# Optimization experiments

Hardware: AMD Instinct MI355X
Metric: run time of the kernel (lower is better)

## Reference

```python
import jax, jax.numpy as jnp
import numpy as np

D = 2048           # model dim
E = 8              # num experts
K = 2              # top_k
H = int(D * 8 / 3) # SwiGLU hidden dim (5461), matches torch default
B, S = 2, 2048


def setup_inputs() -> dict:
    key = jax.random.key(0)
    ks = jax.random.split(key, 5)
    x = jax.random.normal(ks[0], (B, S, D), jnp.float32)
    wg = jax.random.normal(ks[1], (E, D), jnp.float32) * 0.02   # gate Linear weight [out,in]
    w1 = jax.random.normal(ks[2], (E, H, D), jnp.float32) * 0.02  # per-expert w1 [H,D]
    w2 = jax.random.normal(ks[3], (E, D, H), jnp.float32) * 0.02  # per-expert w2 [D,H]
    w3 = jax.random.normal(ks[4], (E, H, D), jnp.float32) * 0.02  # per-expert w3 [H,D]
    return {"x": x, "wg": wg, "w1": w1, "w2": w2, "w3": w3}


def reference(x, wg, w1, w2, w3):
    b, s, d = x.shape
    xf = x.reshape(-1, d)                         # [T, D]
    T = xf.shape[0]

    # --- gating (eval mode: no noise) ---
    logits = xf @ wg.T                            # [T, E]
    topk_vals, topk_idx = jax.lax.top_k(logits, K)  # [T, K]
    topk_probs = jax.nn.softmax(topk_vals, axis=-1)  # softmax over the K selected
    gate_probs = jax.nn.softmax(logits, axis=-1)     # [T, E] for load-balancing loss
    mean_probs = gate_probs.mean(axis=0)             # [E]
    # torch .std() is unbiased (ddof=1)
    lb_loss = (jnp.std(mean_probs, ddof=1) / (mean_probs.mean() + 1e-10)) ** 2

    # --- combine weights: scatter top-k probs into dense [T, E] ---
    cw = jnp.zeros((T, E), xf.dtype).at[jnp.arange(T)[:, None], topk_idx].add(topk_probs)

    # --- per-expert SwiGLU over all tokens (dense grouped GEMMs) ---
    h = jax.nn.silu(jnp.einsum('td,ehd->eth', xf, w1)) * jnp.einsum('td,ehd->eth', xf, w3)
    ye = jnp.einsum('eth,edh->etd', h, w2)        # [E, T, D]

    # --- weighted combine ---
    out = jnp.einsum('etd,te->td', ye, cw).reshape(b, s, d)
    return out, 0.01 * lb_loss
```

## Files before the change

### kernel.cpp

```cpp
#include <hip/hip_runtime.h>
#include <hip/hip_bf16.h>

#define Tn 4096
#define Dm 2048
#define En 8
#define Hh 5461
#define HP 5504

typedef __attribute__((ext_vector_type(8))) short bf16x8;
typedef __attribute__((ext_vector_type(4))) float f32x4;

__device__ __forceinline__ unsigned short f2bf(float f) {
  union { __hip_bfloat16 b; unsigned short u; } c;
  c.b = __float2bfloat16(f);
  return c.u;
}

__device__ __forceinline__ uint4 pack8(const float* f) {
  union { unsigned short us[8]; uint4 v; } o;
#pragma unroll
  for (int i = 0; i < 8; ++i) o.us[i] = f2bf(f[i]);
  return o.v;
}

__device__ __forceinline__ void gl16(const void* g, void* lds) {
  __builtin_amdgcn_global_load_lds(
      (const __attribute__((address_space(1))) unsigned int*)g,
      (__attribute__((address_space(3))) unsigned int*)lds, 16, 0, 0);
}

#define WAIT8_BAR() asm volatile("s_waitcnt vmcnt(8)\n\ts_barrier" ::: "memory")
#define WAIT6_BAR() asm volatile("s_waitcnt vmcnt(6)\n\ts_barrier" ::: "memory")
#define WAIT0_BAR() asm volatile("s_waitcnt vmcnt(0)\n\ts_barrier" ::: "memory")
#define LGK0_BAR()  asm volatile("s_waitcnt lgkmcnt(0)\n\ts_barrier" ::: "memory")


__global__ __launch_bounds__(64) void gating_kernel(
    const float* __restrict__ x, const float* __restrict__ wg,
    float* __restrict__ gate_p, int* __restrict__ topk_e, float* __restrict__ topk_p,
    unsigned short* __restrict__ xb)
{
  const int t = blockIdx.x;
  const int l = threadIdx.x;
  const float* xr = x + (size_t)t * Dm;
  float acc[En];
#pragma unroll
  for (int e = 0; e < En; ++e) acc[e] = 0.f;
  for (int d = l; d < Dm; d += 64) {
    const float xv = xr[d];
#pragma unroll
    for (int e = 0; e < En; ++e) acc[e] = fmaf(xv, wg[e * Dm + d], acc[e]);
  }
#pragma unroll
  for (int e = 0; e < En; ++e) {
    float v = acc[e];
#pragma unroll
    for (int s = 32; s > 0; s >>= 1) v += __shfl_xor(v, s);
    acc[e] = v;
  }
  unsigned short* xrow = xb + (size_t)t * Dm;
#pragma unroll
  for (int k = 0; k < 4; ++k) {
    const int b = k * 512 + l * 8;
    float f[8];
    *(float4*)(f)     = *(const float4*)(xr + b);
    *(float4*)(f + 4) = *(const float4*)(xr + b + 4);
    *(uint4*)(xrow + b) = pack8(f);
  }
  if (l == 0) {
    float m = acc[0];
    for (int e = 1; e < En; ++e) m = fmaxf(m, acc[e]);
    float p[En]; float s = 0.f;
    for (int e = 0; e < En; ++e) { p[e] = __expf(acc[e] - m); s += p[e]; }
    const float inv = 1.f / s;
    for (int e = 0; e < En; ++e) gate_p[t * En + e] = p[e] * inv;
    int e0 = 0; float v0 = acc[0];
    for (int e = 1; e < En; ++e) if (acc[e] > v0) { v0 = acc[e]; e0 = e; }
    int e1 = -1; float v1 = -3.4e38f;
    for (int e = 0; e < En; ++e) if (e != e0 && acc[e] > v1) { v1 = acc[e]; e1 = e; }
    const float q  = __expf(v1 - v0);
    const float q0 = 1.f / (1.f + q);
    const float q1 = q * q0;
    topk_e[t * 2] = e0; topk_e[t * 2 + 1] = e1;
    topk_p[t * 2] = q0; topk_p[t * 2 + 1] = q1;
  }
}

__global__ __launch_bounds__(256) void reduce_scatter_kernel(
    const int* __restrict__ topk_e, const float* __restrict__ topk_p,
    const float* __restrict__ gate_p,
    int* __restrict__ counts, int* __restrict__ offs,
    int* __restrict__ pair_token, int* __restrict__ slot_of,
    float* __restrict__ out_scalar)
{
  __shared__ int cnt_s[En];
  __shared__ int run_s[En];
  __shared__ float red[256 * En];
  const int tid = threadIdx.x;
  if (tid < En) cnt_s[tid] = 0;
  __syncthreads();
  for (int i = tid; i < Tn * 2; i += 256) atomicAdd(&cnt_s[topk_e[i]], 1);
  __syncthreads();
  if (tid == 0) {
    int o = 0;
    for (int e = 0; e < En; ++e) {
      offs[e] = o; run_s[e] = o; counts[e] = cnt_s[e]; o += cnt_s[e];
    }
  }
  __syncthreads();
  for (int i = tid; i < Tn * 2; i += 256) {
    const int e = topk_e[i];
    const int slot = atomicAdd(&run_s[e], 1);
    pair_token[slot] = i >> 1;
    slot_of[i] = slot;
  }
  float p8[En];
#pragma unroll
  for (int e = 0; e < En; ++e) p8[e] = 0.f;
  for (int t = tid; t < Tn; t += 256)
#pragma unroll
    for (int e = 0; e < En; ++e) p8[e] += gate_p[t * En + e];
#pragma unroll
  for (int e = 0; e < En; ++e) red[tid * En + e] = p8[e];
  __syncthreads();
  for (int s = 128; s > 0; s >>= 1) {
    if (tid < s)
#pragma unroll
      for (int e = 0; e < En; ++e) red[tid * En + e] += red[(tid + s) * En + e];
    __syncthreads();
  }
  if (tid == 0) {
    double mp[En]; double sum = 0.0;
    for (int e = 0; e < En; ++e) { mp[e] = (double)red[e] / (double)Tn; sum += mp[e]; }
    const double mean = sum / En;
    double var = 0.0;
    for (int e = 0; e < En; ++e) { const double d = mp[e] - mean; var += d * d; }
    var /= (En - 1);
    const double denom = mean + 1e-10;
    *out_scalar = (float)(0.01 * var / (denom * denom));
  }
}

__global__ __launch_bounds__(256) void cvt_w13_kernel(
    const float* __restrict__ w1, const float* __restrict__ w3,
    unsigned short* __restrict__ w1b, unsigned short* __restrict__ w3b)
{
  const float* src = blockIdx.y ? w3 : w1;
  unsigned short* dst = blockIdx.y ? w3b : w1b;
  const unsigned i = ((unsigned)blockIdx.x * 256u + threadIdx.x) * 8u;
  const unsigned per_e = (unsigned)HP * Dm;
  const unsigned e = i / per_e;
  const unsigned r = i % per_e;
  const unsigned row = r / Dm, col = r % Dm;
  uint4 v;
  if (row < Hh) {
    const float* s = src + (size_t)e * Hh * Dm + (size_t)row * Dm + col;
    float f[8];
    *(float4*)(f)     = *(const float4*)(s);
    *(float4*)(f + 4) = *(const float4*)(s + 4);
    v = pack8(f);
  } else {
    v = (uint4){0, 0, 0, 0};
  }
  *(uint4*)(dst + i) = v;
}

__global__ __launch_bounds__(256) void cvt_w2_kernel(const float* __restrict__ w2,
                                                     unsigned short* __restrict__ w2b)
{
  const unsigned i = ((unsigned)blockIdx.x * 256u + threadIdx.x) * 8u;
  const unsigned per_e = (unsigned)Dm * HP;
  const unsigned e = i / per_e;
  const unsigned r = i % per_e;
  const unsigned row = r / HP, col = r % HP;
  const float* s = w2 + (size_t)e * Dm * Hh + (size_t)row * Hh + col;
  float f[8];
#pragma unroll
  for (int k = 0; k < 8; ++k) f[k] = (col + k < Hh) ? s[k] : 0.f;
  *(uint4*)(w2b + i) = pack8(f);
}

__global__ __launch_bounds__(256, 2) void gemm1_kernel(
    const unsigned short* __restrict__ xb,
    const unsigned short* __restrict__ w1b, const unsigned short* __restrict__ w3b,
    const int* __restrict__ counts, const int* __restrict__ offs,
    const int* __restrict__ pair_token,
    unsigned short* __restrict__ h)
{
  const int bid = blockIdx.x;
  const int logical = (bid & 7) * 344 + (bid >> 3);
  const int z  = logical & 7;
  const int pe = logical >> 3;
  const int e  = pe & 7;
  const int jp = pe >> 3;

  const int cnt = counts[e];
  if (cnt <= 0) return;
  const int base = offs[e];
  const int j0 = jp * 128;
  const int tid = threadIdx.x;
  const int l = tid & 63;
  const int wid = tid >> 6;
  const int wr = wid >> 1, wc = wid & 1;

  __shared__ unsigned short As[2][128 * 32];
  __shared__ unsigned short B1[2][128 * 32];
  __shared__ unsigned short B3[2][128 * 32];

  const int r0 = tid >> 2;
  const int r1 = 64 + (tid >> 2);
  const int c0 = (((tid & 3) ^ ((tid >> 3) & 3))) * 8;
  const int wb0 = wid * 512;
  const int wb1 = 2048 + wid * 512;

  const unsigned short* b1r0 = w1b + ((size_t)e * HP + j0 + r0) * Dm + c0;
  const unsigned short* b1r1 = w1b + ((size_t)e * HP + j0 + r1) * Dm + c0;
  const unsigned short* b3r0 = w3b + ((size_t)e * HP + j0 + r0) * Dm + c0;
  const unsigned short* b3r1 = w3b + ((size_t)e * HP + j0 + r1) * Dm + c0;

  const int lr = l & 15;
  const int sq = (((l >> 4) ^ ((lr >> 1) & 3))) * 8;

#define STAGE1(b, kk) do { \
    gl16(a0 + (kk), &As[b][wb0]);   gl16(a1 + (kk), &As[b][wb1]); \
    gl16(b1r0 + (kk), &B1[b][wb0]); gl16(b1r1 + (kk), &B1[b][wb1]); \
    gl16(b3r0 + (kk), &B3[b][wb0]); gl16(b3r1 + (kk), &B3[b][wb1]); \
  } while (0)

#define COMPUTE1(b) do { \
    bf16x8 av[4], b1v[4], b3v[4]; \
    _Pragma("unroll") \
    for (int m = 0; m < 4; ++m) \
      av[m] = *(const bf16x8*)(&As[b][(wr * 64 + m * 16 + lr) * 32 + sq]); \
    _Pragma("unroll") \
    for (int n = 0; n < 4; ++n) { \
      b1v[n] = *(const bf16x8*)(&B1[b][(wc * 64 + n * 16 + lr) * 32 + sq]); \
      b3v[n] = *(const bf16x8*)(&B3[b][(wc * 64 + n * 16 + lr) * 32 + sq]); \
    } \
    _Pragma("unroll") \
    for (int m = 0; m < 4; ++m) \
      _Pragma("unroll") \
      for (int n = 0; n < 4; ++n) { \
        acc1[m][n] = __builtin_amdgcn_mfma_f32_16x16x32_bf16(av[m], b1v[n], acc1[m][n], 0, 0, 0); \
        acc3[m][n] = __builtin_amdgcn_mfma_f32_16x16x32_bf16(av[m], b3v[n], acc3[m][n], 0, 0, 0); \
      } \
  } while (0)

  for (int mt = z; mt * 128 < cnt; mt += 8) {
    const int row0 = mt * 128;
    int s0 = row0 + r0; if (s0 >= cnt) s0 = cnt - 1;
    int s1 = row0 + r1; if (s1 >= cnt) s1 = cnt - 1;
    const unsigned short* a0 = xb + (size_t)pair_token[base + s0] * Dm + c0;
    const unsigned short* a1 = xb + (size_t)pair_token[base + s1] * Dm + c0;

    f32x4 acc1[4][4], acc3[4][4];
#pragma unroll
    for (int m = 0; m < 4; ++m)
#pragma unroll
      for (int n = 0; n < 4; ++n) {
        acc1[m][n] = (f32x4){0.f, 0.f, 0.f, 0.f};
        acc3[m][n] = (f32x4){0.f, 0.f, 0.f, 0.f};
      }

    STAGE1(0, 0);
    int cur = 0;
    for (int kk = 0; kk < Dm - 32; kk += 32) {
      STAGE1(cur ^ 1, kk + 32);
      WAIT6_BAR();
      COMPUTE1(cur);
      LGK0_BAR();
      cur ^= 1;
    }
    WAIT0_BAR();
    COMPUTE1(cur);
    LGK0_BAR();

#pragma unroll
    for (int m = 0; m < 4; ++m) {
      const int rb = wr * 64 + m * 16 + ((l >> 4) << 2);
#pragma unroll
      for (int i = 0; i < 4; ++i) {
        const int sl2 = row0 + rb + i;
        if (sl2 < cnt) {
          unsigned short* hrow = h + (size_t)(base + sl2) * HP + j0 + wc * 64 + lr;
#pragma unroll
          for (int n = 0; n < 4; ++n) {
            const float aa = acc1[m][n][i];
            const float g = aa / (1.f + __expf(-aa));
            hrow[n * 16] = f2bf(g * acc3[m][n][i]);
          }
        }
      }
    }
  }
#undef STAGE1
#undef COMPUTE1
}

__global__ __launch_bounds__(256, 2) void gemm2_kernel(
    const unsigned short* __restrict__ h, const unsigned short* __restrict__ w2b,
    const int* __restrict__ counts, const int* __restrict__ offs,
    float* __restrict__ y)
{
  const int bid = blockIdx.x;
  const int logical = (bid & 7) * 128 + (bid >> 3);
  const int z  = logical & 7;
  const int pe = logical >> 3;
  const int e  = pe & 7;
  const int dp = pe >> 3;

  const int cnt = counts[e];
  if (cnt <= 0) return;
  const int base = offs[e];
  const int d0 = dp * 128;
  const int tid = threadIdx.x;
  const int l = tid & 63;
  const int wid = tid >> 6;
  const int wr = wid >> 1, wc = wid & 1;

  __shared__ unsigned short Ah[2][128 * 64];
  __shared__ unsigned short Bs[2][128 * 64];

  const int r0 = tid >> 3;
  const int c0 = (((tid & 7) ^ ((tid >> 3) & 7))) * 8;

  const unsigned short* br0 = w2b + ((size_t)e * Dm + d0 + r0)      * HP + c0;
  const unsigned short* br1 = w2b + ((size_t)e * Dm + d0 + r0 + 32) * HP + c0;
  const unsigned short* br2 = w2b + ((size_t)e * Dm + d0 + r0 + 64) * HP + c0;
  const unsigned short* br3 = w2b + ((size_t)e * Dm + d0 + r0 + 96) * HP + c0;

  const int wbA0 = (0 * 256 + wid * 64) * 8;
  const int wbA1 = (1 * 256 + wid * 64) * 8;
  const int wbA2 = (2 * 256 + wid * 64) * 8;
  const int wbA3 = (3 * 256 + wid * 64) * 8;

  const int lr = l & 15;
  const int sq0 = (((0 * 4 + (l >> 4)) ^ (lr & 7))) * 8;
  const int sq1 = (((1 * 4 + (l >> 4)) ^ (lr & 7))) * 8;

#define STAGE2(b, kk) do { \
    gl16(a0 + (kk), &Ah[b][wbA0]); gl16(a1 + (kk), &Ah[b][wbA1]); \
    gl16(a2 + (kk), &Ah[b][wbA2]); gl16(a3 + (kk), &Ah[b][wbA3]); \
    gl16(br0 + (kk), &Bs[b][wbA0]); gl16(br1 + (kk), &Bs[b][wbA1]); \
    gl16(br2 + (kk), &Bs[b][wbA2]); gl16(br3 + (kk), &Bs[b][wbA3]); \
  } while (0)

#define COMPUTE2(b) do { \
    bf16x8 av[4], bv[4]; \
    _Pragma("unroll") \
    for (int m = 0; m < 4; ++m) \
      av[m] = *(const bf16x8*)(&Ah[b][(wr * 64 + m * 16 + lr) * 64 + sq0]); \
    _Pragma("unroll") \
    for (int n = 0; n < 4; ++n) \
      bv[n] = *(const bf16x8*)(&Bs[b][(wc * 64 + n * 16 + lr) * 64 + sq0]); \
    _Pragma("unroll") \
    for (int m = 0; m < 4; ++m) \
      _Pragma("unroll") \
      for (int n = 0; n < 4; ++n) \
        acc[m][n] = __builtin_amdgcn_mfma_f32_16x16x32_bf16(av[m], bv[n], acc[m][n], 0, 0, 0); \
    _Pragma("unroll") \
    for (int m = 0; m < 4; ++m) \
      av[m] = *(const bf16x8*)(&Ah[b][(wr * 64 + m * 16 + lr) * 64 + sq1]); \
    _Pragma("unroll") \
    for (int n = 0; n < 4; ++n) \
      bv[n] = *(const bf16x8*)(&Bs[b][(wc * 64 + n * 16 + lr) * 64 + sq1]); \
    _Pragma("unroll") \
    for (int m = 0; m < 4; ++m) \
      _Pragma("unroll") \
      for (int n = 0; n < 4; ++n) \
        acc[m][n] = __builtin_amdgcn_mfma_f32_16x16x32_bf16(av[m], bv[n], acc[m][n], 0, 0, 0); \
  } while (0)

  for (int mt = z; mt * 128 < cnt; mt += 8) {
    const int row0 = mt * 128;
    int s0 = row0 + r0;      if (s0 >= cnt) s0 = cnt - 1;
    int s1 = row0 + r0 + 32; if (s1 >= cnt) s1 = cnt - 1;
    int s2 = row0 + r0 + 64; if (s2 >= cnt) s2 = cnt - 1;
    int s3 = row0 + r0 + 96; if (s3 >= cnt) s3 = cnt - 1;
    const unsigned short* a0 = h + (size_t)(base + s0) * HP + c0;
    const unsigned short* a1 = h + (size_t)(base + s1) * HP + c0;
    const unsigned short* a2 = h + (size_t)(base + s2) * HP + c0;
    const unsigned short* a3 = h + (size_t)(base + s3) * HP + c0;

    f32x4 acc[4][4];
#pragma unroll
    for (int m = 0; m < 4; ++m)
#pragma unroll
      for (int n = 0; n < 4; ++n) acc[m][n] = (f32x4){0.f, 0.f, 0.f, 0.f};

    STAGE2(0, 0);
    int cur = 0;
    for (int kk = 0; kk < HP - 64; kk += 64) {
      STAGE2(cur ^ 1, kk + 64);
      WAIT8_BAR();
      COMPUTE2(cur);
      LGK0_BAR();
      cur ^= 1;
    }
    WAIT0_BAR();
    COMPUTE2(cur);
    LGK0_BAR();

#pragma unroll
    for (int m = 0; m < 4; ++m) {
      const int rb = row0 + wr * 64 + m * 16 + ((l >> 4) << 2);
#pragma unroll
      for (int i = 0; i < 4; ++i) {
        const int sl2 = rb + i;
        if (sl2 < cnt) {
          float* yrow = y + (size_t)(base + sl2) * Dm + d0 + wc * 64 + lr;
#pragma unroll
          for (int n = 0; n < 4; ++n)
            yrow[n * 16] = acc[m][n][i];
        }
      }
    }
  }
#undef STAGE2
#undef COMPUTE2
}

__global__ __launch_bounds__(256) void combine_kernel(
    const float* __restrict__ y, const int* __restrict__ slot_of,
    const float* __restrict__ topk_p, float* __restrict__ out)
{
  const int t = blockIdx.x;
  const int s0 = slot_of[t * 2], s1 = slot_of[t * 2 + 1];
  const float w0 = topk_p[t * 2], w1 = topk_p[t * 2 + 1];
  const float* y0 = y + (size_t)s0 * Dm;
  const float* y1 = y + (size_t)s1 * Dm;
  float* o = out + (size_t)t * Dm;
  const int c = threadIdx.x * 8;
  float4 a0 = *(const float4*)(y0 + c);
  float4 a1 = *(const float4*)(y0 + c + 4);
  float4 b0 = *(const float4*)(y1 + c);
  float4 b1 = *(const float4*)(y1 + c + 4);
  float4 r0, r1;
  r0.x = w0 * a0.x + w1 * b0.x; r0.y = w0 * a0.y + w1 * b0.y;
  r0.z = w0 * a0.z + w1 * b0.z; r0.w = w0 * a0.w + w1 * b0.w;
  r1.x = w0 * a1.x + w1 * b1.x; r1.y = w0 * a1.y + w1 * b1.y;
  r1.z = w0 * a1.z + w1 * b1.z; r1.w = w0 * a1.w + w1 * b1.w;
  *(float4*)(o + c) = r0;
  *(float4*)(o + c + 4) = r1;
}

extern "C" void kernel_launch(void* const* d_in, const int* in_sizes, int n_in,
                              void* d_out, int out_size, void* d_ws, size_t ws_size,
                              hipStream_t stream) {
  const float* x  = (const float*)d_in[0];
  const float* wg = (const float*)d_in[1];
  const float* w1 = (const float*)d_in[2];
  const float* w2 = (const float*)d_in[3];
  const float* w3 = (const float*)d_in[4];
  float* out = (float*)d_out;

  char* ws = (char*)d_ws;
  int*    counts     = (int*)(ws + 64);
  int*    offs       = (int*)(ws + 128);
  int*    topk_e     = (int*)(ws + 1024);
  float*  topk_p     = (float*)(ws + 40960);
  int*    pair_token = (int*)(ws + 81920);
  float*  gate_p     = (float*)(ws + 163840);
  int*    slot_of    = (int*)(ws + 307200);
  const size_t MB = 1u << 20;
  unsigned short* xb  = (unsigned short*)(ws + 1 * MB);
  unsigned short* h   = (unsigned short*)(ws + 17 * MB);
  unsigned short* w1b = (unsigned short*)(ws + 104 * MB);
  unsigned short* w3b = (unsigned short*)(ws + 276 * MB);
  unsigned short* w2b = (unsigned short*)(ws + 448 * MB);
  float* y = (float*)(ws + 104 * MB);

  gating_kernel  <<<Tn, 64, 0, stream>>>(x, wg, gate_p, topk_e, topk_p, xb);
  reduce_scatter_kernel<<<1, 256, 0, stream>>>(topk_e, topk_p, gate_p, counts, offs,
                                               pair_token, slot_of, out + (size_t)Tn * Dm);
  cvt_w13_kernel <<<dim3(En * HP * Dm / 8 / 256, 2), 256, 0, stream>>>(w1, w3, w1b, w3b);
  cvt_w2_kernel  <<<En * Dm * HP / 8 / 256, 256, 0, stream>>>(w2, w2b);
  gemm1_kernel   <<<43 * En * 8, 256, 0, stream>>>(xb, w1b, w3b, counts, offs, pair_token, h);
  gemm2_kernel   <<<(Dm / 128) * En * 8, 256, 0, stream>>>(h, w2b, counts, offs, y);
  combine_kernel <<<Tn, 256, 0, stream>>>(y, slot_of, topk_p, out);
}
```

Before: 1.464 ms.

## Restructure gemm1 into 8-wave 256-row tiles with triple-buffered phased MFMA schedule

gemm1 moves from 4 waves on a 128x128 tile to 8 waves on a 256x128 tile, so each loaded weight tile is reused across twice as many token rows. The shared-memory pipeline goes from double to triple buffering with a two-stage prefetch. Each k-step is split into four phases of LDS reads and MFMAs separated by barriers, with s_setprio raising priority around the MFMA bursts so waves interleave memory and matrix work. The cost is more LDS per block, more barriers per k-step and fewer blocks in the grid, which can hurt occupancy and load balance across experts with uneven token counts.

```diff
diff --git a/kernel.cpp b/kernel.cpp
--- a/kernel.cpp
+++ b/kernel.cpp
@@ -31,8 +31,11 @@
 
 #define WAIT8_BAR() asm volatile("s_waitcnt vmcnt(8)\n\ts_barrier" ::: "memory")
 #define WAIT6_BAR() asm volatile("s_waitcnt vmcnt(6)\n\ts_barrier" ::: "memory")
+#define WAIT4_BAR() asm volatile("s_waitcnt vmcnt(4)\n\ts_barrier" ::: "memory")
 #define WAIT0_BAR() asm volatile("s_waitcnt vmcnt(0)\n\ts_barrier" ::: "memory")
 #define LGK0_BAR()  asm volatile("s_waitcnt lgkmcnt(0)\n\ts_barrier" ::: "memory")
+#define BAR_LGK0()  asm volatile("s_barrier\n\ts_waitcnt lgkmcnt(0)" ::: "memory")
+#define BARP()      asm volatile("s_barrier" ::: "memory")
 
 
 __global__ __launch_bounds__(64) void gating_kernel(
@@ -180,7 +183,7 @@
   *(uint4*)(w2b + i) = pack8(f);
 }
 
-__global__ __launch_bounds__(256, 2) void gemm1_kernel(
+__global__ __launch_bounds__(512, 2) void gemm1_kernel(
     const unsigned short* __restrict__ xb,
     const unsigned short* __restrict__ w1b, const unsigned short* __restrict__ w3b,
     const int* __restrict__ counts, const int* __restrict__ offs,
@@ -188,9 +191,9 @@
     unsigned short* __restrict__ h)
 {
   const int bid = blockIdx.x;
-  const int logical = (bid & 7) * 344 + (bid >> 3);
-  const int z  = logical & 7;
-  const int pe = logical >> 3;
+  const int logical = (bid & 7) * 172 + (bid >> 3);
+  const int z  = logical & 3;
+  const int pe = logical >> 2;
   const int e  = pe & 7;
   const int jp = pe >> 3;
 
@@ -201,57 +204,99 @@
   const int tid = threadIdx.x;
   const int l = tid & 63;
   const int wid = tid >> 6;
-  const int wr = wid >> 1, wc = wid & 1;
-
-  __shared__ unsigned short As[2][128 * 32];
-  __shared__ unsigned short B1[2][128 * 32];
-  __shared__ unsigned short B3[2][128 * 32];
+  const int wr = wid & 3;
+  const int wc = wid >> 2;
+
+  __shared__ unsigned short As[3][256 * 32];
+  __shared__ unsigned short B1s[3][128 * 32];
+  __shared__ unsigned short B3s[3][128 * 32];
 
   const int r0 = tid >> 2;
-  const int r1 = 64 + (tid >> 2);
   const int c0 = (((tid & 3) ^ ((tid >> 3) & 3))) * 8;
-  const int wb0 = wid * 512;
-  const int wb1 = 2048 + wid * 512;
-
-  const unsigned short* b1r0 = w1b + ((size_t)e * HP + j0 + r0) * Dm + c0;
-  const unsigned short* b1r1 = w1b + ((size_t)e * HP + j0 + r1) * Dm + c0;
-  const unsigned short* b3r0 = w3b + ((size_t)e * HP + j0 + r0) * Dm + c0;
-  const unsigned short* b3r1 = w3b + ((size_t)e * HP + j0 + r1) * Dm + c0;
+  const int wbA0 = wid * 512;
+  const int wbA1 = 4096 + wid * 512;
+  const int wbB  = wid * 512;
+
+  const unsigned short* b1g = w1b + ((size_t)e * HP + j0 + r0) * Dm + c0;
+  const unsigned short* b3g = w3b + ((size_t)e * HP + j0 + r0) * Dm + c0;
 
   const int lr = l & 15;
   const int sq = (((l >> 4) ^ ((lr >> 1) & 3))) * 8;
 
-#define STAGE1(b, kk) do { \
-    gl16(a0 + (kk), &As[b][wb0]);   gl16(a1 + (kk), &As[b][wb1]); \
-    gl16(b1r0 + (kk), &B1[b][wb0]); gl16(b1r1 + (kk), &B1[b][wb1]); \
-    gl16(b3r0 + (kk), &B3[b][wb0]); gl16(b3r1 + (kk), &B3[b][wb1]); \
+#define STG(b, kk) do { \
+    gl16(a0g + (kk), &As[b][wbA0]); gl16(a1g + (kk), &As[b][wbA1]); \
+    gl16(b1g + (kk), &B1s[b][wbB]); gl16(b3g + (kk), &B3s[b][wbB]); \
   } while (0)
 
-#define COMPUTE1(b) do { \
-    bf16x8 av[4], b1v[4], b3v[4]; \
-    _Pragma("unroll") \
-    for (int m = 0; m < 4; ++m) \
-      av[m] = *(const bf16x8*)(&As[b][(wr * 64 + m * 16 + lr) * 32 + sq]); \
-    _Pragma("unroll") \
-    for (int n = 0; n < 4; ++n) { \
-      b1v[n] = *(const bf16x8*)(&B1[b][(wc * 64 + n * 16 + lr) * 32 + sq]); \
-      b3v[n] = *(const bf16x8*)(&B3[b][(wc * 64 + n * 16 + lr) * 32 + sq]); \
-    } \
-    _Pragma("unroll") \
-    for (int m = 0; m < 4; ++m) \
-      _Pragma("unroll") \
-      for (int n = 0; n < 4; ++n) { \
-        acc1[m][n] = __builtin_amdgcn_mfma_f32_16x16x32_bf16(av[m], b1v[n], acc1[m][n], 0, 0, 0); \
-        acc3[m][n] = __builtin_amdgcn_mfma_f32_16x16x32_bf16(av[m], b3v[n], acc3[m][n], 0, 0, 0); \
-      } \
+#define PHASES(b) do { \
+    bf16x8 av0 = *(const bf16x8*)(&As[b][(wr * 64 +  0 + lr) * 32 + sq]); \
+    bf16x8 av1 = *(const bf16x8*)(&As[b][(wr * 64 + 16 + lr) * 32 + sq]); \
+    bf16x8 av2 = *(const bf16x8*)(&As[b][(wr * 64 + 32 + lr) * 32 + sq]); \
+    bf16x8 av3 = *(const bf16x8*)(&As[b][(wr * 64 + 48 + lr) * 32 + sq]); \
+    bf16x8 t0 = *(const bf16x8*)(&B1s[b][(wc * 64 +  0 + lr) * 32 + sq]); \
+    bf16x8 t1 = *(const bf16x8*)(&B1s[b][(wc * 64 + 16 + lr) * 32 + sq]); \
+    BAR_LGK0(); \
+    __builtin_amdgcn_s_setprio(1); \
+    acc1[0][0] = __builtin_amdgcn_mfma_f32_16x16x32_bf16(av0, t0, acc1[0][0], 0, 0, 0); \
+    acc1[1][0] = __builtin_amdgcn_mfma_f32_16x16x32_bf16(av1, t0, acc1[1][0], 0, 0, 0); \
+    acc1[2][0] = __builtin_amdgcn_mfma_f32_16x16x32_bf16(av2, t0, acc1[2][0], 0, 0, 0); \
+    acc1[3][0] = __builtin_amdgcn_mfma_f32_16x16x32_bf16(av3, t0, acc1[3][0], 0, 0, 0); \
+    acc1[0][1] = __builtin_amdgcn_mfma_f32_16x16x32_bf16(av0, t1, acc1[0][1], 0, 0, 0); \
+    acc1[1][1] = __builtin_amdgcn_mfma_f32_16x16x32_bf16(av1, t1, acc1[1][1], 0, 0, 0); \
+    acc1[2][1] = __builtin_amdgcn_mfma_f32_16x16x32_bf16(av2, t1, acc1[2][1], 0, 0, 0); \
+    acc1[3][1] = __builtin_amdgcn_mfma_f32_16x16x32_bf16(av3, t1, acc1[3][1], 0, 0, 0); \
+    __builtin_amdgcn_s_setprio(0); \
+    BARP(); \
+    t0 = *(const bf16x8*)(&B3s[b][(wc * 64 +  0 + lr) * 32 + sq]); \
+    t1 = *(const bf16x8*)(&B3s[b][(wc * 64 + 16 + lr) * 32 + sq]); \
+    BAR_LGK0(); \
+    __builtin_amdgcn_s_setprio(1); \
+    acc3[0][0] = __builtin_amdgcn_mfma_f32_16x16x32_bf16(av0, t0, acc3[0][0], 0, 0, 0); \
+    acc3[1][0] = __builtin_amdgcn_mfma_f32_16x16x32_bf16(av1, t0, acc3[1][0], 0, 0, 0); \
+    acc3[2][0] = __builtin_amdgcn_mfma_f32_16x16x32_bf16(av2, t0, acc3[2][0], 0, 0, 0); \
+    acc3[3][0] = __builtin_amdgcn_mfma_f32_16x16x32_bf16(av3, t0, acc3[3][0], 0, 0, 0); \
+    acc3[0][1] = __builtin_amdgcn_mfma_f32_16x16x32_bf16(av0, t1, acc3[0][1], 0, 0, 0); \
+    acc3[1][1] = __builtin_amdgcn_mfma_f32_16x16x32_bf16(av1, t1, acc3[1][1], 0, 0, 0); \
+    acc3[2][1] = __builtin_amdgcn_mfma_f32_16x16x32_bf16(av2, t1, acc3[2][1], 0, 0, 0); \
+    acc3[3][1] = __builtin_amdgcn_mfma_f32_16x16x32_bf16(av3, t1, acc3[3][1], 0, 0, 0); \
+    __builtin_amdgcn_s_setprio(0); \
+    BARP(); \
+    t0 = *(const bf16x8*)(&B1s[b][(wc * 64 + 32 + lr) * 32 + sq]); \
+    t1 = *(const bf16x8*)(&B1s[b][(wc * 64 + 48 + lr) * 32 + sq]); \
+    BAR_LGK0(); \
+    __builtin_amdgcn_s_setprio(1); \
+    acc1[0][2] = __builtin_amdgcn_mfma_f32_16x16x32_bf16(av0, t0, acc1[0][2], 0, 0, 0); \
+    acc1[1][2] = __builtin_amdgcn_mfma_f32_16x16x32_bf16(av1, t0, acc1[1][2], 0, 0, 0); \
+    acc1[2][2] = __builtin_amdgcn_mfma_f32_16x16x32_bf16(av2, t0, acc1[2][2], 0, 0, 0); \
+    acc1[3][2] = __builtin_amdgcn_mfma_f32_16x16x32_bf16(av3, t0, acc1[3][2], 0, 0, 0); \
+    acc1[0][3] = __builtin_amdgcn_mfma_f32_16x16x32_bf16(av0, t1, acc1[0][3], 0, 0, 0); \
+    acc1[1][3] = __builtin_amdgcn_mfma_f32_16x16x32_bf16(av1, t1, acc1[1][3], 0, 0, 0); \
+    acc1[2][3] = __builtin_amdgcn_mfma_f32_16x16x32_bf16(av2, t1, acc1[2][3], 0, 0, 0); \
+    acc1[3][3] = __builtin_amdgcn_mfma_f32_16x16x32_bf16(av3, t1, acc1[3][3], 0, 0, 0); \
+    __builtin_amdgcn_s_setprio(0); \
+    BARP(); \
+    t0 = *(const bf16x8*)(&B3s[b][(wc * 64 + 32 + lr) * 32 + sq]); \
+    t1 = *(const bf16x8*)(&B3s[b][(wc * 64 + 48 + lr) * 32 + sq]); \
+    BAR_LGK0(); \
+    __builtin_amdgcn_s_setprio(1); \
+    acc3[0][2] = __builtin_amdgcn_mfma_f32_16x16x32_bf16(av0, t0, acc3[0][2], 0, 0, 0); \
+    acc3[1][2] = __builtin_amdgcn_mfma_f32_16x16x32_bf16(av1, t0, acc3[1][2], 0, 0, 0); \
+    acc3[2][2] = __builtin_amdgcn_mfma_f32_16x16x32_bf16(av2, t0, acc3[2][2], 0, 0, 0); \
+    acc3[3][2] = __builtin_amdgcn_mfma_f32_16x16x32_bf16(av3, t0, acc3[3][2], 0, 0, 0); \
+    acc3[0][3] = __builtin_amdgcn_mfma_f32_16x16x32_bf16(av0, t1, acc3[0][3], 0, 0, 0); \
+    acc3[1][3] = __builtin_amdgcn_mfma_f32_16x16x32_bf16(av1, t1, acc3[1][3], 0, 0, 0); \
+    acc3[2][3] = __builtin_amdgcn_mfma_f32_16x16x32_bf16(av2, t1, acc3[2][3], 0, 0, 0); \
+    acc3[3][3] = __builtin_amdgcn_mfma_f32_16x16x32_bf16(av3, t1, acc3[3][3], 0, 0, 0); \
+    __builtin_amdgcn_s_setprio(0); \
+    BARP(); \
   } while (0)
 
-  for (int mt = z; mt * 128 < cnt; mt += 8) {
-    const int row0 = mt * 128;
-    int s0 = row0 + r0; if (s0 >= cnt) s0 = cnt - 1;
-    int s1 = row0 + r1; if (s1 >= cnt) s1 = cnt - 1;
-    const unsigned short* a0 = xb + (size_t)pair_token[base + s0] * Dm + c0;
-    const unsigned short* a1 = xb + (size_t)pair_token[base + s1] * Dm + c0;
+  for (int mt = z; mt * 256 < cnt; mt += 4) {
+    const int row0 = mt * 256;
+    int s0 = row0 + r0;       if (s0 >= cnt) s0 = cnt - 1;
+    int s1 = row0 + 128 + r0; if (s1 >= cnt) s1 = cnt - 1;
+    const unsigned short* a0g = xb + (size_t)pair_token[base + s0] * Dm + c0;
+    const unsigned short* a1g = xb + (size_t)pair_token[base + s1] * Dm + c0;
 
     f32x4 acc1[4][4], acc3[4][4];
 #pragma unroll
@@ -262,18 +307,21 @@
         acc3[m][n] = (f32x4){0.f, 0.f, 0.f, 0.f};
       }
 
-    STAGE1(0, 0);
+    STG(0, 0);
+    STG(1, 32);
     int cur = 0;
-    for (int kk = 0; kk < Dm - 32; kk += 32) {
-      STAGE1(cur ^ 1, kk + 32);
-      WAIT6_BAR();
-      COMPUTE1(cur);
-      LGK0_BAR();
-      cur ^= 1;
+    for (int t = 0; t < 62; ++t) {
+      int sb = cur + 2; if (sb >= 3) sb -= 3;
+      STG(sb, (t + 2) * 32);
+      WAIT8_BAR();
+      PHASES(cur);
+      cur = (cur == 2) ? 0 : cur + 1;
     }
+    WAIT4_BAR();
+    PHASES(cur);
+    cur = (cur == 2) ? 0 : cur + 1;
     WAIT0_BAR();
-    COMPUTE1(cur);
-    LGK0_BAR();
+    PHASES(cur);
 
 #pragma unroll
     for (int m = 0; m < 4; ++m) {
@@ -293,8 +341,8 @@
       }
     }
   }
-#undef STAGE1
-#undef COMPUTE1
+#undef STG
+#undef PHASES
 }
 
 __global__ __launch_bounds__(256, 2) void gemm2_kernel(
@@ -475,7 +523,7 @@
                                                pair_token, slot_of, out + (size_t)Tn * Dm);
   cvt_w13_kernel <<<dim3(En * HP * Dm / 8 / 256, 2), 256, 0, stream>>>(w1, w3, w1b, w3b);
   cvt_w2_kernel  <<<En * Dm * HP / 8 / 256, 256, 0, stream>>>(w2, w2b);
-  gemm1_kernel   <<<43 * En * 8, 256, 0, stream>>>(xb, w1b, w3b, counts, offs, pair_token, h);
+  gemm1_kernel   <<<43 * En * 4, 512, 0, stream>>>(xb, w1b, w3b, counts, offs, pair_token, h);
   gemm2_kernel   <<<(Dm / 128) * En * 8, 256, 0, stream>>>(h, w2b, counts, offs, y);
   combine_kernel <<<Tn, 256, 0, stream>>>(y, slot_of, topk_p, out);
 }
```

Result: slower. 1.695 ms (+15.8%).

## Fuse w1/w3 bf16 conversion into gemm1 by staging fp32 weights in LDS

Applied to the files above, without the earlier changes.

Drops the separate kernel that converted w1 and w3 from fp32 to padded bf16 copies. gemm1 now streams the fp32 weights straight into LDS with swizzled global-to-LDS loads and converts them to bf16 while building the MFMA fragments. Padded hidden columns are zeroed at the h store instead. This removes a full pass that read both fp32 weight tensors and wrote their bf16 copies. In exchange gemm1 fetches twice as many weight bytes per tile, uses more LDS (which may limit occupancy), and spends extra VALU work on conversion in its inner loop.

```diff
diff --git a/kernel.cpp b/kernel.cpp
--- a/kernel.cpp
+++ b/kernel.cpp
@@ -23,16 +23,23 @@
   return o.v;
 }
 
+__device__ __forceinline__ bf16x8 cvt8(float4 a, float4 b) {
+  union { unsigned short us[8]; bf16x8 v; } o;
+  o.us[0] = f2bf(a.x); o.us[1] = f2bf(a.y); o.us[2] = f2bf(a.z); o.us[3] = f2bf(a.w);
+  o.us[4] = f2bf(b.x); o.us[5] = f2bf(b.y); o.us[6] = f2bf(b.z); o.us[7] = f2bf(b.w);
+  return o.v;
+}
+
 __device__ __forceinline__ void gl16(const void* g, void* lds) {
   __builtin_amdgcn_global_load_lds(
       (const __attribute__((address_space(1))) unsigned int*)g,
       (__attribute__((address_space(3))) unsigned int*)lds, 16, 0, 0);
 }
 
-#define WAIT8_BAR() asm volatile("s_waitcnt vmcnt(8)\n\ts_barrier" ::: "memory")
-#define WAIT6_BAR() asm volatile("s_waitcnt vmcnt(6)\n\ts_barrier" ::: "memory")
-#define WAIT0_BAR() asm volatile("s_waitcnt vmcnt(0)\n\ts_barrier" ::: "memory")
-#define LGK0_BAR()  asm volatile("s_waitcnt lgkmcnt(0)\n\ts_barrier" ::: "memory")
+#define WAIT10_BAR() asm volatile("s_waitcnt vmcnt(10)\n\ts_barrier" ::: "memory")
+#define WAIT8_BAR()  asm volatile("s_waitcnt vmcnt(8)\n\ts_barrier" ::: "memory")
+#define WAIT0_BAR()  asm volatile("s_waitcnt vmcnt(0)\n\ts_barrier" ::: "memory")
+#define LGK0_BAR()   asm volatile("s_waitcnt lgkmcnt(0)\n\ts_barrier" ::: "memory")
 
 
 __global__ __launch_bounds__(64) void gating_kernel(
@@ -141,30 +148,6 @@
   }
 }
 
-__global__ __launch_bounds__(256) void cvt_w13_kernel(
-    const float* __restrict__ w1, const float* __restrict__ w3,
-    unsigned short* __restrict__ w1b, unsigned short* __restrict__ w3b)
-{
-  const float* src = blockIdx.y ? w3 : w1;
-  unsigned short* dst = blockIdx.y ? w3b : w1b;
-  const unsigned i = ((unsigned)blockIdx.x * 256u + threadIdx.x) * 8u;
-  const unsigned per_e = (unsigned)HP * Dm;
-  const unsigned e = i / per_e;
-  const unsigned r = i % per_e;
-  const unsigned row = r / Dm, col = r % Dm;
-  uint4 v;
-  if (row < Hh) {
-    const float* s = src + (size_t)e * Hh * Dm + (size_t)row * Dm + col;
-    float f[8];
-    *(float4*)(f)     = *(const float4*)(s);
-    *(float4*)(f + 4) = *(const float4*)(s + 4);
-    v = pack8(f);
-  } else {
-    v = (uint4){0, 0, 0, 0};
-  }
-  *(uint4*)(dst + i) = v;
-}
-
 __global__ __launch_bounds__(256) void cvt_w2_kernel(const float* __restrict__ w2,
                                                      unsigned short* __restrict__ w2b)
 {
@@ -182,7 +165,7 @@
 
 __global__ __launch_bounds__(256, 2) void gemm1_kernel(
     const unsigned short* __restrict__ xb,
-    const unsigned short* __restrict__ w1b, const unsigned short* __restrict__ w3b,
+    const float* __restrict__ w1, const float* __restrict__ w3,
     const int* __restrict__ counts, const int* __restrict__ offs,
     const int* __restrict__ pair_token,
     unsigned short* __restrict__ h)
@@ -204,38 +187,61 @@
   const int wr = wid >> 1, wc = wid & 1;
 
   __shared__ unsigned short As[2][128 * 32];
-  __shared__ unsigned short B1[2][128 * 32];
-  __shared__ unsigned short B3[2][128 * 32];
-
-  const int r0 = tid >> 2;
-  const int r1 = 64 + (tid >> 2);
-  const int c0 = (((tid & 3) ^ ((tid >> 3) & 3))) * 8;
-  const int wb0 = wid * 512;
-  const int wb1 = 2048 + wid * 512;
-
-  const unsigned short* b1r0 = w1b + ((size_t)e * HP + j0 + r0) * Dm + c0;
-  const unsigned short* b1r1 = w1b + ((size_t)e * HP + j0 + r1) * Dm + c0;
-  const unsigned short* b3r0 = w3b + ((size_t)e * HP + j0 + r0) * Dm + c0;
-  const unsigned short* b3r1 = w3b + ((size_t)e * HP + j0 + r1) * Dm + c0;
+  __shared__ float B1f[2][128 * 32];
+  __shared__ float B3f[2][128 * 32];
+
+  const int rA0 = tid >> 2;
+  const int cA0 = (((tid & 3) ^ ((tid >> 3) & 3))) * 8;
+  const int wbA0 = wid * 512;
+  const int wbA1 = 2048 + wid * 512;
+
+  const int rBl = tid >> 3;
+  const int cBf = (((tid & 7) ^ ((tid >> 3) & 7))) * 4;
+  int rB0 = j0 + rBl;      if (rB0 >= Hh) rB0 = Hh - 1;
+  int rB1 = j0 + 32 + rBl; if (rB1 >= Hh) rB1 = Hh - 1;
+  int rB2 = j0 + 64 + rBl; if (rB2 >= Hh) rB2 = Hh - 1;
+  int rB3 = j0 + 96 + rBl; if (rB3 >= Hh) rB3 = Hh - 1;
+  const float* b1g0 = w1 + ((size_t)e * Hh + rB0) * Dm + cBf;
+  const float* b1g1 = w1 + ((size_t)e * Hh + rB1) * Dm + cBf;
+  const float* b1g2 = w1 + ((size_t)e * Hh + rB2) * Dm + cBf;
+  const float* b1g3 = w1 + ((size_t)e * Hh + rB3) * Dm + cBf;
+  const float* b3g0 = w3 + ((size_t)e * Hh + rB0) * Dm + cBf;
+  const float* b3g1 = w3 + ((size_t)e * Hh + rB1) * Dm + cBf;
+  const float* b3g2 = w3 + ((size_t)e * Hh + rB2) * Dm + cBf;
+  const float* b3g3 = w3 + ((size_t)e * Hh + rB3) * Dm + cBf;
+  const int wbF0 = (0 * 256 + wid * 64) * 4;
+  const int wbF1 = (1 * 256 + wid * 64) * 4;
+  const int wbF2 = (2 * 256 + wid * 64) * 4;
+  const int wbF3 = (3 * 256 + wid * 64) * 4;
 
   const int lr = l & 15;
-  const int sq = (((l >> 4) ^ ((lr >> 1) & 3))) * 8;
+  const int sqA = (((l >> 4) ^ ((lr >> 1) & 3))) * 8;
+  const int qB  = 2 * (l >> 4);
+  const int pB0 = ((qB)     ^ (lr & 7)) * 4;
+  const int pB1 = ((qB + 1) ^ (lr & 7)) * 4;
 
 #define STAGE1(b, kk) do { \
-    gl16(a0 + (kk), &As[b][wb0]);   gl16(a1 + (kk), &As[b][wb1]); \
-    gl16(b1r0 + (kk), &B1[b][wb0]); gl16(b1r1 + (kk), &B1[b][wb1]); \
-    gl16(b3r0 + (kk), &B3[b][wb0]); gl16(b3r1 + (kk), &B3[b][wb1]); \
+    gl16(a0g + (kk), &As[b][wbA0]);  gl16(a1g + (kk), &As[b][wbA1]); \
+    gl16(b1g0 + (kk), &B1f[b][wbF0]); gl16(b1g1 + (kk), &B1f[b][wbF1]); \
+    gl16(b1g2 + (kk), &B1f[b][wbF2]); gl16(b1g3 + (kk), &B1f[b][wbF3]); \
+    gl16(b3g0 + (kk), &B3f[b][wbF0]); gl16(b3g1 + (kk), &B3f[b][wbF1]); \
+    gl16(b3g2 + (kk), &B3f[b][wbF2]); gl16(b3g3 + (kk), &B3f[b][wbF3]); \
   } while (0)
 
 #define COMPUTE1(b) do { \
     bf16x8 av[4], b1v[4], b3v[4]; \
     _Pragma("unroll") \
     for (int m = 0; m < 4; ++m) \
-      av[m] = *(const bf16x8*)(&As[b][(wr * 64 + m * 16 + lr) * 32 + sq]); \
+      av[m] = *(const bf16x8*)(&As[b][(wr * 64 + m * 16 + lr) * 32 + sqA]); \
     _Pragma("unroll") \
     for (int n = 0; n < 4; ++n) { \
-      b1v[n] = *(const bf16x8*)(&B1[b][(wc * 64 + n * 16 + lr) * 32 + sq]); \
-      b3v[n] = *(const bf16x8*)(&B3[b][(wc * 64 + n * 16 + lr) * 32 + sq]); \
+      const int rw = (wc * 64 + n * 16 + lr) * 32; \
+      float4 f0 = *(const float4*)(&B1f[b][rw + pB0]); \
+      float4 f1 = *(const float4*)(&B1f[b][rw + pB1]); \
+      b1v[n] = cvt8(f0, f1); \
+      f0 = *(const float4*)(&B3f[b][rw + pB0]); \
+      f1 = *(const float4*)(&B3f[b][rw + pB1]); \
+      b3v[n] = cvt8(f0, f1); \
     } \
     _Pragma("unroll") \
     for (int m = 0; m < 4; ++m) \
@@ -248,10 +254,10 @@
 
   for (int mt = z; mt * 128 < cnt; mt += 8) {
     const int row0 = mt * 128;
-    int s0 = row0 + r0; if (s0 >= cnt) s0 = cnt - 1;
-    int s1 = row0 + r1; if (s1 >= cnt) s1 = cnt - 1;
-    const unsigned short* a0 = xb + (size_t)pair_token[base + s0] * Dm + c0;
-    const unsigned short* a1 = xb + (size_t)pair_token[base + s1] * Dm + c0;
+    int s0 = row0 + rA0;      if (s0 >= cnt) s0 = cnt - 1;
+    int s1 = row0 + 64 + rA0; if (s1 >= cnt) s1 = cnt - 1;
+    const unsigned short* a0g = xb + (size_t)pair_token[base + s0] * Dm + cA0;
+    const unsigned short* a1g = xb + (size_t)pair_token[base + s1] * Dm + cA0;
 
     f32x4 acc1[4][4], acc3[4][4];
 #pragma unroll
@@ -266,7 +272,7 @@
     int cur = 0;
     for (int kk = 0; kk < Dm - 32; kk += 32) {
       STAGE1(cur ^ 1, kk + 32);
-      WAIT6_BAR();
+      WAIT10_BAR();
       COMPUTE1(cur);
       LGK0_BAR();
       cur ^= 1;
@@ -275,6 +281,7 @@
     COMPUTE1(cur);
     LGK0_BAR();
 
+    const int colb = j0 + wc * 64 + lr;
 #pragma unroll
     for (int m = 0; m < 4; ++m) {
       const int rb = wr * 64 + m * 16 + ((l >> 4) << 2);
@@ -282,12 +289,13 @@
       for (int i = 0; i < 4; ++i) {
         const int sl2 = row0 + rb + i;
         if (sl2 < cnt) {
-          unsigned short* hrow = h + (size_t)(base + sl2) * HP + j0 + wc * 64 + lr;
+          unsigned short* hrow = h + (size_t)(base + sl2) * HP + colb;
 #pragma unroll
           for (int n = 0; n < 4; ++n) {
             const float aa = acc1[m][n][i];
             const float g = aa / (1.f + __expf(-aa));
-            hrow[n * 16] = f2bf(g * acc3[m][n][i]);
+            const float hv = (colb + n * 16 < Hh) ? g * acc3[m][n][i] : 0.f;
+            hrow[n * 16] = f2bf(hv);
           }
         }
       }
@@ -465,17 +473,14 @@
   const size_t MB = 1u << 20;
   unsigned short* xb  = (unsigned short*)(ws + 1 * MB);
   unsigned short* h   = (unsigned short*)(ws + 17 * MB);
-  unsigned short* w1b = (unsigned short*)(ws + 104 * MB);
-  unsigned short* w3b = (unsigned short*)(ws + 276 * MB);
   unsigned short* w2b = (unsigned short*)(ws + 448 * MB);
   float* y = (float*)(ws + 104 * MB);
 
   gating_kernel  <<<Tn, 64, 0, stream>>>(x, wg, gate_p, topk_e, topk_p, xb);
   reduce_scatter_kernel<<<1, 256, 0, stream>>>(topk_e, topk_p, gate_p, counts, offs,
                                                pair_token, slot_of, out + (size_t)Tn * Dm);
-  cvt_w13_kernel <<<dim3(En * HP * Dm / 8 / 256, 2), 256, 0, stream>>>(w1, w3, w1b, w3b);
   cvt_w2_kernel  <<<En * Dm * HP / 8 / 256, 256, 0, stream>>>(w2, w2b);
-  gemm1_kernel   <<<43 * En * 8, 256, 0, stream>>>(xb, w1b, w3b, counts, offs, pair_token, h);
+  gemm1_kernel   <<<43 * En * 8, 256, 0, stream>>>(xb, w1, w3, counts, offs, pair_token, h);
   gemm2_kernel   <<<(Dm / 128) * En * 8, 256, 0, stream>>>(h, w2b, counts, offs, y);
   combine_kernel <<<Tn, 256, 0, stream>>>(y, slot_of, topk_p, out);
 }
```

New measurement: 1.569 ms. +7.2%, slower.
